# Optimization experiments

Measured on AMD Instinct MI355X. Metric: run time of the kernel, lower is better.

The kernel has to match this reference:

```python
import jax, jax.numpy as jnp
import numpy as np

B, T, D_IN, H, N_LAYERS, D_OUT = 256, 512, 128, 512, 3, 1


def setup_inputs() -> dict:
    key = jax.random.key(0)
    ks = jax.random.split(key, 20)
    s = 1.0 / np.sqrt(H)
    inp = {"x": jax.random.normal(ks[0], (B, T, D_IN), dtype=jnp.float32)}
    k = 1
    for l in range(N_LAYERS):
        d_in = D_IN if l == 0 else H
        inp[f"W_ih_{l}"] = jax.random.uniform(ks[k], (4 * H, d_in), minval=-s, maxval=s); k += 1
        inp[f"W_hh_{l}"] = jax.random.uniform(ks[k], (4 * H, H), minval=-s, maxval=s); k += 1
        inp[f"b_ih_{l}"] = jax.random.uniform(ks[k], (4 * H,), minval=-s, maxval=s); k += 1
        inp[f"b_hh_{l}"] = jax.random.uniform(ks[k], (4 * H,), minval=-s, maxval=s); k += 1
    inp["W_fc"] = jax.random.uniform(ks[k], (D_OUT, H), minval=-s, maxval=s); k += 1
    inp["b_fc"] = jax.random.uniform(ks[k], (D_OUT,), minval=-s, maxval=s)
    return inp


def _lstm_layer(x, W_ih, W_hh, b_ih, b_hh):
    # x: [B, T, d_in] -> hs: [B, T, H]. PyTorch gate order: i, f, g, o.
    xg = jnp.einsum("btd,gd->btg", x, W_ih) + b_ih + b_hh  # precompute input proj [B,T,4H]
    Hh = W_hh.shape[1]
    Bb = x.shape[0]

    def step(carry, xg_t):
        h, c = carry
        g = xg_t + h @ W_hh.T  # [B, 4H]
        i, f, gg, o = jnp.split(g, 4, axis=-1)
        c = jax.nn.sigmoid(f) * c + jax.nn.sigmoid(i) * jnp.tanh(gg)
        h = jax.nn.sigmoid(o) * jnp.tanh(c)
        return (h, c), h

    h0 = jnp.zeros((Bb, Hh), x.dtype)
    (_, _), hs = jax.lax.scan(step, (h0, h0), jnp.swapaxes(xg, 0, 1))
    return jnp.swapaxes(hs, 0, 1)


def reference(x, W_ih_0, W_hh_0, b_ih_0, b_hh_0,
              W_ih_1, W_hh_1, b_ih_1, b_hh_1,
              W_ih_2, W_hh_2, b_ih_2, b_hh_2,
              W_fc, b_fc):
    # Eval mode: inter-layer dropout (p=0.4) is identity.
    h = _lstm_layer(x, W_ih_0, W_hh_0, b_ih_0, b_hh_0)
    h = _lstm_layer(h, W_ih_1, W_hh_1, b_ih_1, b_hh_1)
    h = _lstm_layer(h, W_ih_2, W_hh_2, b_ih_2, b_hh_2)
    return h[:, -1, :] @ W_fc.T + b_fc  # [B, D_OUT]
```

## Files before the change

### kernel.cpp

```cpp
#include <hip/hip_runtime.h>

#define B_   256
#define T_   512
#define DIN_ 128
#define H_   512
#define G4_  2048

typedef __bf16 bf16_t;
typedef __bf16 bf16x8 __attribute__((ext_vector_type(8)));
typedef __bf16 bf16x4 __attribute__((ext_vector_type(4)));
typedef float  f32x4  __attribute__((ext_vector_type(4)));
typedef float  f32x16 __attribute__((ext_vector_type(16)));

__device__ __forceinline__ void gload16cc(const void* g, void* l) {
  __builtin_amdgcn_global_load_lds(
      (const __attribute__((address_space(1))) unsigned int*)g,
      (__attribute__((address_space(3))) unsigned int*)l, 16, 0, 17);
}

__global__ void cast_f32_bf16(const float* __restrict__ s, bf16_t* __restrict__ d, int n) {
  int i = (blockIdx.x * 256 + threadIdx.x) * 4;
  if (i >= n) return;
  float4 v = *(const float4*)(s + i);
  bf16x4 o;
  o[0] = (bf16_t)v.x; o[1] = (bf16_t)v.y; o[2] = (bf16_t)v.z; o[3] = (bf16_t)v.w;
  *(bf16x4*)(d + i) = o;
}

__global__ void cast_strided(const float* __restrict__ s, bf16_t* __restrict__ d,
                             int Ks, int Kd, int coff) {
  int npr = Ks >> 3;
  int i = blockIdx.x * 256 + threadIdx.x;
  if (i >= 2048 * npr) return;
  int row = i / npr, j = i - row * npr;
  const float* sp = s + (size_t)row * Ks + j * 8;
  float4 v0 = *(const float4*)sp;
  float4 v1 = *(const float4*)(sp + 4);
  bf16x8 o;
  o[0] = (bf16_t)v0.x; o[1] = (bf16_t)v0.y; o[2] = (bf16_t)v0.z; o[3] = (bf16_t)v0.w;
  o[4] = (bf16_t)v1.x; o[5] = (bf16_t)v1.y; o[6] = (bf16_t)v1.z; o[7] = (bf16_t)v1.w;
  *(bf16x8*)(d + (size_t)row * Kd + coff + j * 8) = o;
}

__global__ void bias_sum(const float* __restrict__ a, const float* __restrict__ b,
                         float* __restrict__ o, int n) {
  int i = blockIdx.x * 256 + threadIdx.x;
  if (i < n) o[i] = a[i] + b[i];
}

#define RING_N (8 * 256 * 512)
#define FSTR   16

template<bool L0>
__device__ __forceinline__ void step_loop(
    char* smem, const bf16_t* __restrict__ xbf, const bf16_t* __restrict__ wcl,
    const float* __restrict__ bias_l, bf16_t* ringPrev, bf16_t* ringOwn,
    float* __restrict__ hsf, int* flags, int layer, int bg, int ug)
{
  constexpr int KL   = L0 ? 640 : 1024;
  constexpr int ROWB = KL * 2;
  constexpr int XT   = L0 ? 4 : 16;
  constexpr int HT   = 16;
  constexpr int XP1  = L0 ? 2 : 8;
  constexpr int HOFF = L0 ? 256 : 1024;
  const int tid  = threadIdx.x;
  const int lane = tid & 63;
  const int wv   = tid >> 6;
  const int g    = wv & 3;
  const int kh   = wv >> 2;
  const int r32  = lane & 31;
  const int l5   = lane >> 5;
  const int u0   = ug * 32;
  const int t0x  = L0 ? (kh * 4) : (kh * 16);
  const int t0h  = L0 ? (8 + kh * 16) : (32 + kh * 16);

  bf16x8 wfrag[XT + HT];
  {
    const bf16_t* wrow = wcl + (size_t)(g * 512 + u0 + r32) * KL + l5 * 8;
    #pragma unroll
    for (int i = 0; i < XT; ++i) wfrag[i]      = *(const bf16x8*)(wrow + (t0x + i) * 16);
    #pragma unroll
    for (int i = 0; i < HT; ++i) wfrag[XT + i] = *(const bf16x8*)(wrow + (t0h + i) * 16);
  }
  const int um = tid >> 3;
  const int uq = tid & 7;
  float bsv[4][4];
  #pragma unroll
  for (int g2 = 0; g2 < 4; ++g2)
    #pragma unroll
    for (int q = 0; q < 4; ++q)
      bsv[g2][q] = bias_l[g2 * 512 + u0 + uq * 4 + q];

  float cst[4] = {0.f, 0.f, 0.f, 0.f};
  float* gp = (float*)smem;

  int* fl_own  = flags + ((layer * 512) * 4 + bg) * FSTR;
  int* fl_prev = flags + (((layer - 1) * 512) * 4 + bg) * FSTR;
  int* fl_next = flags + (((layer + 1) * 512) * 4 + bg) * FSTR;

  for (int s = 0; s < 512; ++s) {
    const int slot  = s & 7;
    const int slot2 = (s - 1) & 7;
    if (!L0) {
      if (tid == 0)
        while (__hip_atomic_load(fl_prev + s * 4 * FSTR, __ATOMIC_RELAXED,
                                 __HIP_MEMORY_SCOPE_AGENT) < 16)
          __builtin_amdgcn_s_sleep(1);
      __syncthreads();
      const bf16_t* prvS = ringPrev + (size_t)slot * (256 * 512) + (size_t)(bg * 64) * 512;
      #pragma unroll
      for (int i = 0; i < 8; ++i) {
        int r = i * 8 + wv;
        gload16cc(prvS + r * 512 + (lane ^ (r & 15)) * 8, smem + r * ROWB);
      }
    } else {
      #pragma unroll
      for (int i2 = 0; i2 < 2; ++i2) {
        int idx = i2 * 512 + tid;
        int r = idx >> 4, cx = idx & 15;
        int px = cx ^ (r & 15);
        bf16x8 v = *(const bf16x8*)(xbf + ((size_t)(bg * 64 + r) * T_ + s) * 128 + cx * 8);
        *(bf16x8*)(smem + r * ROWB + px * 16) = v;
      }
    }
    __syncthreads();
    f32x16 acc0 = {}, acc1 = {};
    #pragma unroll
    for (int i = 0; i < XP1; ++i) {
      const int px = ((t0x + i) * 2 + l5) ^ (r32 & 15);
      bf16x8 a0 = *(const bf16x8*)(smem + r32 * ROWB + px * 16);
      bf16x8 a1 = *(const bf16x8*)(smem + (32 + r32) * ROWB + px * 16);
      acc0 = __builtin_amdgcn_mfma_f32_32x32x16_bf16(a0, wfrag[i], acc0, 0, 0, 0);
      acc1 = __builtin_amdgcn_mfma_f32_32x32x16_bf16(a1, wfrag[i], acc1, 0, 0, 0);
    }
    if (tid == 0) {
      if (s > 0)
        while (__hip_atomic_load(fl_own + (s - 1) * 4 * FSTR, __ATOMIC_RELAXED,
                                 __HIP_MEMORY_SCOPE_AGENT) < 16)
          __builtin_amdgcn_s_sleep(1);
      if (layer < 2 && s >= 8)
        while (__hip_atomic_load(fl_next + (s - 8) * 4 * FSTR, __ATOMIC_RELAXED,
                                 __HIP_MEMORY_SCOPE_AGENT) < 16)
          __builtin_amdgcn_s_sleep(1);
    }
    __syncthreads();
    {
      const bf16_t* ownS = ringOwn + (size_t)slot2 * (256 * 512) + (size_t)(bg * 64) * 512;
      #pragma unroll
      for (int i = 0; i < 8; ++i) {
        int r = i * 8 + wv;
        gload16cc(ownS + r * 512 + (lane ^ (r & 15)) * 8, smem + r * ROWB + HOFF);
      }
    }
    #pragma unroll
    for (int i = XP1; i < XT; ++i) {
      const int px = ((t0x + i) * 2 + l5) ^ (r32 & 15);
      bf16x8 a0 = *(const bf16x8*)(smem + r32 * ROWB + px * 16);
      bf16x8 a1 = *(const bf16x8*)(smem + (32 + r32) * ROWB + px * 16);
      acc0 = __builtin_amdgcn_mfma_f32_32x32x16_bf16(a0, wfrag[i], acc0, 0, 0, 0);
      acc1 = __builtin_amdgcn_mfma_f32_32x32x16_bf16(a1, wfrag[i], acc1, 0, 0, 0);
    }
    __syncthreads();
    #pragma unroll
    for (int i = 0; i < HT; ++i) {
      const int px = ((t0h + i) * 2 + l5) ^ (r32 & 15);
      bf16x8 a0 = *(const bf16x8*)(smem + r32 * ROWB + px * 16);
      bf16x8 a1 = *(const bf16x8*)(smem + (32 + r32) * ROWB + px * 16);
      acc0 = __builtin_amdgcn_mfma_f32_32x32x16_bf16(a0, wfrag[XT + i], acc0, 0, 0, 0);
      acc1 = __builtin_amdgcn_mfma_f32_32x32x16_bf16(a1, wfrag[XT + i], acc1, 0, 0, 0);
    }
    __syncthreads();
    {
      const int base = kh * 8192 + g * 32 + r32;
      #pragma unroll
      for (int reg = 0; reg < 16; ++reg) {
        int mr = (reg & 3) + 8 * (reg >> 2) + 4 * l5;
        gp[base + mr * 128]        = acc0[reg];
        gp[base + (32 + mr) * 128] = acc1[reg];
      }
    }
    __syncthreads();
    union { bf16x4 v; unsigned long long u; } pk;
    f32x4 hvf;
    {
      f32x4 gv[4];
      #pragma unroll
      for (int g2 = 0; g2 < 4; ++g2) {
        f32x4 p0 = *(const f32x4*)&gp[um * 128 + g2 * 32 + uq * 4];
        f32x4 p1 = *(const f32x4*)&gp[8192 + um * 128 + g2 * 32 + uq * 4];
        #pragma unroll
        for (int q = 0; q < 4; ++q) gv[g2][q] = p0[q] + p1[q];
      }
      #pragma unroll
      for (int q = 0; q < 4; ++q) {
        float i_ = gv[0][q] + bsv[0][q];
        float f_ = gv[1][q] + bsv[1][q];
        float g_ = gv[2][q] + bsv[2][q];
        float o_ = gv[3][q] + bsv[3][q];
        float si = 1.f / (1.f + __expf(-i_));
        float sf = 1.f / (1.f + __expf(-f_));
        float so = 1.f / (1.f + __expf(-o_));
        float tg = 2.f / (1.f + __expf(-2.f * g_)) - 1.f;
        float cv = sf * cst[q] + si * tg;
        cst[q] = cv;
        float th = 2.f / (1.f + __expf(-2.f * cv)) - 1.f;
        hvf[q] = so * th;
        pk.v[q] = (bf16_t)hvf[q];
      }
    }
    {
      int b = bg * 64 + um;
      bf16_t* dst = ringOwn + (size_t)slot * (256 * 512) + (size_t)b * 512 + u0 + uq * 4;
      (void)__hip_atomic_exchange((unsigned long long*)dst, pk.u,
                                  __ATOMIC_RELAXED, __HIP_MEMORY_SCOPE_AGENT);
      if (layer == 2 && s == 511)
        *(f32x4*)(hsf + (size_t)b * 512 + u0 + uq * 4) = hvf;
    }
    __syncthreads();
    if (tid == 0)
      atomicAdd(fl_own + s * 4 * FSTR, 1);
  }
}

__global__ __launch_bounds__(512, 2)
void lstm_persist(const bf16_t* __restrict__ xbf, const bf16_t* __restrict__ wc,
                  const float* __restrict__ bias, bf16_t* __restrict__ rings,
                  float* __restrict__ hsf, int* __restrict__ flags)
{
  __shared__ __align__(16) char smem[131072];
  const int bid   = blockIdx.x;
  const int layer = bid >> 6;
  const int bg    = (bid >> 4) & 3;
  const int ug    = bid & 15;
  bf16_t* ringOwn  = rings + (size_t)layer * RING_N;
  bf16_t* ringPrev = rings + (size_t)(layer - 1) * RING_N;
  if (layer == 0) {
    step_loop<true>(smem, xbf, wc, bias, ringPrev, ringOwn, hsf, flags, 0, bg, ug);
  } else {
    const bf16_t* wcl = wc + 2048 * 640 + (size_t)(layer - 1) * 2048 * 1024;
    step_loop<false>(smem, xbf, wcl, bias + layer * 2048, ringPrev, ringOwn, hsf,
                     flags, layer, bg, ug);
  }
}

__global__ void fc_kernel(const float* __restrict__ h, const float* __restrict__ Wfc,
                          const float* __restrict__ bfc, float* __restrict__ out) {
  int b = blockIdx.x;
  int l = threadIdx.x;
  const float* hp = h + (size_t)b * H_;
  float acc = 0.f;
  #pragma unroll
  for (int i = 0; i < 8; ++i) acc += hp[l + i * 64] * Wfc[l + i * 64];
  #pragma unroll
  for (int off = 32; off; off >>= 1) acc += __shfl_down(acc, off, 64);
  if (l == 0) out[b] = acc + bfc[0];
}

extern "C" void kernel_launch(void* const* d_in, const int* in_sizes, int n_in,
                              void* d_out, int out_size, void* d_ws, size_t ws_size,
                              hipStream_t stream) {
  const float* x        = (const float*)d_in[0];
  const float* Wih_f[3] = {(const float*)d_in[1], (const float*)d_in[5], (const float*)d_in[9]};
  const float* Whh_f[3] = {(const float*)d_in[2], (const float*)d_in[6], (const float*)d_in[10]};
  const float* bih_f[3] = {(const float*)d_in[3], (const float*)d_in[7], (const float*)d_in[11]};
  const float* bhh_f[3] = {(const float*)d_in[4], (const float*)d_in[8], (const float*)d_in[12]};
  const float* Wfc = (const float*)d_in[13];
  const float* bfc = (const float*)d_in[14];

  char* ws = (char*)d_ws;
  size_t off = 0;
  auto take = [&](size_t bytes) { char* p = ws + off; off = (off + bytes + 255) & ~255ULL; return p; };
  bf16_t* XBF   = (bf16_t*)take((size_t)B_ * T_ * DIN_ * 2);
  bf16_t* WC    = (bf16_t*)take((size_t)(2048*640 + 2*2048*1024) * 2);
  float*  BIAS  = (float*) take(3 * 2048 * 4);
  bf16_t* RINGS = (bf16_t*)take((size_t)3 * RING_N * 2);
  float*  HSF   = (float*) take((size_t)B_ * H_ * 4);
  int*    FLAGS = (int*)   take(3 * 512 * 4 * FSTR * 4);

  bf16_t* WC1 = WC + 2048 * 640;
  bf16_t* WC2 = WC1 + 2048 * 1024;

  cast_f32_bf16<<<16384, 256, 0, stream>>>(x, XBF, B_ * T_ * DIN_);
  cast_strided<<<128, 256, 0, stream>>>(Wih_f[0], WC,  128, 640, 0);
  cast_strided<<<512, 256, 0, stream>>>(Whh_f[0], WC,  512, 640, 128);
  cast_strided<<<512, 256, 0, stream>>>(Wih_f[1], WC1, 512, 1024, 0);
  cast_strided<<<512, 256, 0, stream>>>(Whh_f[1], WC1, 512, 1024, 512);
  cast_strided<<<512, 256, 0, stream>>>(Wih_f[2], WC2, 512, 1024, 0);
  cast_strided<<<512, 256, 0, stream>>>(Whh_f[2], WC2, 512, 1024, 512);
  for (int l = 0; l < 3; ++l)
    bias_sum<<<8, 256, 0, stream>>>(bih_f[l], bhh_f[l], BIAS + l * 2048, G4_);
  hipMemsetAsync(RINGS, 0, (size_t)3 * RING_N * 2, stream);
  hipMemsetAsync(FLAGS, 0, 3 * 512 * 4 * FSTR * 4, stream);

  lstm_persist<<<192, 512, 0, stream>>>(XBF, WC, BIAS, RINGS, HSF, FLAGS);
  fc_kernel<<<B_, 64, 0, stream>>>(HSF, Wfc, bfc, (float*)d_out);
}
```

Before: 3.276 ms.

## Offload layer 1-2 input projections to helper blocks feeding fp32 xg rings

```diff
diff --git a/kernel.cpp b/kernel.cpp
--- a/kernel.cpp
+++ b/kernel.cpp
@@ -16,6 +16,9 @@
   __builtin_amdgcn_global_load_lds(
       (const __attribute__((address_space(1))) unsigned int*)g,
       (__attribute__((address_space(3))) unsigned int*)l, 16, 0, 17);
+}
+__device__ __forceinline__ int fload(const int* p) {
+  return __hip_atomic_load(p, __ATOMIC_RELAXED, __HIP_MEMORY_SCOPE_AGENT);
 }
 
 __global__ void cast_f32_bf16(const float* __restrict__ s, bf16_t* __restrict__ d, int n) {
@@ -49,20 +52,15 @@
 }
 
 #define RING_N (8 * 256 * 512)
+#define XG_N   (8 * 256 * 2048)
 #define FSTR   16
 
-template<bool L0>
-__device__ __forceinline__ void step_loop(
+__device__ __forceinline__ void l0_loop(
     char* smem, const bf16_t* __restrict__ xbf, const bf16_t* __restrict__ wcl,
-    const float* __restrict__ bias_l, bf16_t* ringPrev, bf16_t* ringOwn,
-    float* __restrict__ hsf, int* flags, int layer, int bg, int ug)
+    const float* __restrict__ bias_l, bf16_t* ringOwn, int* flags, int* xgf,
+    int bg, int ug)
 {
-  constexpr int KL   = L0 ? 640 : 1024;
-  constexpr int ROWB = KL * 2;
-  constexpr int XT   = L0 ? 4 : 16;
-  constexpr int HT   = 16;
-  constexpr int XP1  = L0 ? 2 : 8;
-  constexpr int HOFF = L0 ? 256 : 1024;
+  constexpr int ROWB = 1280;
   const int tid  = threadIdx.x;
   const int lane = tid & 63;
   const int wv   = tid >> 6;
@@ -71,16 +69,16 @@
   const int r32  = lane & 31;
   const int l5   = lane >> 5;
   const int u0   = ug * 32;
-  const int t0x  = L0 ? (kh * 4) : (kh * 16);
-  const int t0h  = L0 ? (8 + kh * 16) : (32 + kh * 16);
-
-  bf16x8 wfrag[XT + HT];
+  const int t0x  = kh * 4;
+  const int t0h  = 8 + kh * 16;
+
+  bf16x8 wfrag[20];
   {
-    const bf16_t* wrow = wcl + (size_t)(g * 512 + u0 + r32) * KL + l5 * 8;
-    #pragma unroll
-    for (int i = 0; i < XT; ++i) wfrag[i]      = *(const bf16x8*)(wrow + (t0x + i) * 16);
-    #pragma unroll
-    for (int i = 0; i < HT; ++i) wfrag[XT + i] = *(const bf16x8*)(wrow + (t0h + i) * 16);
+    const bf16_t* wrow = wcl + (size_t)(g * 512 + u0 + r32) * 640 + l5 * 8;
+    #pragma unroll
+    for (int i = 0; i < 4; ++i)  wfrag[i]     = *(const bf16x8*)(wrow + (t0x + i) * 16);
+    #pragma unroll
+    for (int i = 0; i < 16; ++i) wfrag[4 + i] = *(const bf16x8*)(wrow + (t0h + i) * 16);
   }
   const int um = tid >> 3;
   const int uq = tid & 7;
@@ -94,39 +92,24 @@
   float cst[4] = {0.f, 0.f, 0.f, 0.f};
   float* gp = (float*)smem;
 
-  int* fl_own  = flags + ((layer * 512) * 4 + bg) * FSTR;
-  int* fl_prev = flags + (((layer - 1) * 512) * 4 + bg) * FSTR;
-  int* fl_next = flags + (((layer + 1) * 512) * 4 + bg) * FSTR;
+  int* fl_own = flags + (0 * 4 + bg) * FSTR;
+  int* bpf    = xgf + (0 * 4 + bg) * FSTR;
 
   for (int s = 0; s < 512; ++s) {
     const int slot  = s & 7;
     const int slot2 = (s - 1) & 7;
-    if (!L0) {
-      if (tid == 0)
-        while (__hip_atomic_load(fl_prev + s * 4 * FSTR, __ATOMIC_RELAXED,
-                                 __HIP_MEMORY_SCOPE_AGENT) < 16)
-          __builtin_amdgcn_s_sleep(1);
-      __syncthreads();
-      const bf16_t* prvS = ringPrev + (size_t)slot * (256 * 512) + (size_t)(bg * 64) * 512;
-      #pragma unroll
-      for (int i = 0; i < 8; ++i) {
-        int r = i * 8 + wv;
-        gload16cc(prvS + r * 512 + (lane ^ (r & 15)) * 8, smem + r * ROWB);
-      }
-    } else {
-      #pragma unroll
-      for (int i2 = 0; i2 < 2; ++i2) {
-        int idx = i2 * 512 + tid;
-        int r = idx >> 4, cx = idx & 15;
-        int px = cx ^ (r & 15);
-        bf16x8 v = *(const bf16x8*)(xbf + ((size_t)(bg * 64 + r) * T_ + s) * 128 + cx * 8);
-        *(bf16x8*)(smem + r * ROWB + px * 16) = v;
-      }
+    {
+      int r0 = tid >> 4, c0 = tid & 15;
+      bf16x8 v0 = *(const bf16x8*)(xbf + ((size_t)(bg * 64 + r0) * T_ + s) * 128 + c0 * 8);
+      int i1 = 512 + tid, r1 = i1 >> 4, c1 = i1 & 15;
+      bf16x8 v1 = *(const bf16x8*)(xbf + ((size_t)(bg * 64 + r1) * T_ + s) * 128 + c1 * 8);
+      *(bf16x8*)(smem + r0 * ROWB + (c0 ^ (r0 & 15)) * 16) = v0;
+      *(bf16x8*)(smem + r1 * ROWB + (c1 ^ (r1 & 15)) * 16) = v1;
     }
     __syncthreads();
     f32x16 acc0 = {}, acc1 = {};
     #pragma unroll
-    for (int i = 0; i < XP1; ++i) {
+    for (int i = 0; i < 2; ++i) {
       const int px = ((t0x + i) * 2 + l5) ^ (r32 & 15);
       bf16x8 a0 = *(const bf16x8*)(smem + r32 * ROWB + px * 16);
       bf16x8 a1 = *(const bf16x8*)(smem + (32 + r32) * ROWB + px * 16);
@@ -135,13 +118,9 @@
     }
     if (tid == 0) {
       if (s > 0)
-        while (__hip_atomic_load(fl_own + (s - 1) * 4 * FSTR, __ATOMIC_RELAXED,
-                                 __HIP_MEMORY_SCOPE_AGENT) < 16)
-          __builtin_amdgcn_s_sleep(1);
-      if (layer < 2 && s >= 8)
-        while (__hip_atomic_load(fl_next + (s - 8) * 4 * FSTR, __ATOMIC_RELAXED,
-                                 __HIP_MEMORY_SCOPE_AGENT) < 16)
-          __builtin_amdgcn_s_sleep(1);
+        while (fload(fl_own + (s - 1) * 4 * FSTR) < 16) __builtin_amdgcn_s_sleep(1);
+      if (s >= 8)
+        while (fload(bpf + (s - 8) * 4 * FSTR) < 8) __builtin_amdgcn_s_sleep(1);
     }
     __syncthreads();
     {
@@ -149,11 +128,11 @@
       #pragma unroll
       for (int i = 0; i < 8; ++i) {
         int r = i * 8 + wv;
-        gload16cc(ownS + r * 512 + (lane ^ (r & 15)) * 8, smem + r * ROWB + HOFF);
-      }
-    }
-    #pragma unroll
-    for (int i = XP1; i < XT; ++i) {
+        gload16cc(ownS + r * 512 + (lane ^ (r & 15)) * 8, smem + r * ROWB + 256);
+      }
+    }
+    #pragma unroll
+    for (int i = 2; i < 4; ++i) {
       const int px = ((t0x + i) * 2 + l5) ^ (r32 & 15);
       bf16x8 a0 = *(const bf16x8*)(smem + r32 * ROWB + px * 16);
       bf16x8 a1 = *(const bf16x8*)(smem + (32 + r32) * ROWB + px * 16);
@@ -162,12 +141,12 @@
     }
     __syncthreads();
     #pragma unroll
-    for (int i = 0; i < HT; ++i) {
+    for (int i = 0; i < 16; ++i) {
       const int px = ((t0h + i) * 2 + l5) ^ (r32 & 15);
       bf16x8 a0 = *(const bf16x8*)(smem + r32 * ROWB + px * 16);
       bf16x8 a1 = *(const bf16x8*)(smem + (32 + r32) * ROWB + px * 16);
-      acc0 = __builtin_amdgcn_mfma_f32_32x32x16_bf16(a0, wfrag[XT + i], acc0, 0, 0, 0);
-      acc1 = __builtin_amdgcn_mfma_f32_32x32x16_bf16(a1, wfrag[XT + i], acc1, 0, 0, 0);
+      acc0 = __builtin_amdgcn_mfma_f32_32x32x16_bf16(a0, wfrag[4 + i], acc0, 0, 0, 0);
+      acc1 = __builtin_amdgcn_mfma_f32_32x32x16_bf16(a1, wfrag[4 + i], acc1, 0, 0, 0);
     }
     __syncthreads();
     {
@@ -181,7 +160,6 @@
     }
     __syncthreads();
     union { bf16x4 v; unsigned long long u; } pk;
-    f32x4 hvf;
     {
       f32x4 gv[4];
       #pragma unroll
@@ -204,6 +182,131 @@
         float cv = sf * cst[q] + si * tg;
         cst[q] = cv;
         float th = 2.f / (1.f + __expf(-2.f * cv)) - 1.f;
+        pk.v[q] = (bf16_t)(so * th);
+      }
+    }
+    {
+      int b = bg * 64 + um;
+      bf16_t* dst = ringOwn + (size_t)slot * (256 * 512) + (size_t)b * 512 + u0 + uq * 4;
+      (void)__hip_atomic_exchange((unsigned long long*)dst, pk.u,
+                                  __ATOMIC_RELAXED, __HIP_MEMORY_SCOPE_AGENT);
+    }
+    __syncthreads();
+    if (tid == 0) atomicAdd(fl_own + s * 4 * FSTR, 1);
+  }
+}
+
+__device__ __forceinline__ void main_loop(
+    char* smem, const bf16_t* __restrict__ wcl, const float* __restrict__ bias_l,
+    const float* __restrict__ xgRing, bf16_t* ringOwn, float* __restrict__ hsf,
+    int* flags, int* xgf, int layer, int bg, int ug)
+{
+  const int tid  = threadIdx.x;
+  const int lane = tid & 63;
+  const int wv   = tid >> 6;
+  const int g    = wv & 3;
+  const int kh   = wv >> 2;
+  const int r32  = lane & 31;
+  const int l5   = lane >> 5;
+  const int u0   = ug * 32;
+
+  bf16x8 wfrag[16];
+  {
+    const bf16_t* wrow = wcl + (size_t)(g * 512 + u0 + r32) * 1024 + 512 + kh * 256 + l5 * 8;
+    #pragma unroll
+    for (int i = 0; i < 16; ++i) wfrag[i] = *(const bf16x8*)(wrow + i * 16);
+  }
+  const int um = tid >> 3;
+  const int uq = tid & 7;
+  float bsv[4][4];
+  #pragma unroll
+  for (int g2 = 0; g2 < 4; ++g2)
+    #pragma unroll
+    for (int q = 0; q < 4; ++q)
+      bsv[g2][q] = bias_l[g2 * 512 + u0 + uq * 4 + q];
+
+  float cst[4] = {0.f, 0.f, 0.f, 0.f};
+
+  int* fl_own = flags + ((layer * 512) * 4 + bg) * FSTR;
+  int* xgf_in = xgf + (((layer - 1) * 512) * 4 + bg) * FSTR;
+  int* xgf_bp = xgf + ((1 * 512) * 4 + bg) * FSTR;
+
+  for (int s = 0; s < 512; ++s) {
+    const int slot  = s & 7;
+    const int slot2 = (s - 1) & 7;
+    if (tid == 0) {
+      while (fload(xgf_in + s * 4 * FSTR) < 8) __builtin_amdgcn_s_sleep(1);
+      if (s > 0)
+        while (fload(fl_own + (s - 1) * 4 * FSTR) < 16) __builtin_amdgcn_s_sleep(1);
+      if (layer == 1 && s >= 8)
+        while (fload(xgf_bp + (s - 8) * 4 * FSTR) < 8) __builtin_amdgcn_s_sleep(1);
+    }
+    __syncthreads();
+    {
+      const bf16_t* ownS = ringOwn + (size_t)slot2 * (256 * 512) + (size_t)(bg * 64) * 512;
+      #pragma unroll
+      for (int i = 0; i < 8; ++i) {
+        int r = i * 8 + wv;
+        gload16cc(ownS + r * 512 + (lane ^ (r & 15)) * 8, smem + r * 1024);
+      }
+      const float* xgS = xgRing + (size_t)slot * (256 * 2048) + (size_t)(bg * 64) * 2048;
+      #pragma unroll
+      for (int i = 0; i < 4; ++i) {
+        int id = (i * 8 + wv) * 64 + lane;
+        int row = id >> 5, sub = id & 31, g2 = sub >> 3, cp = sub & 7;
+        gload16cc(xgS + (size_t)row * 2048 + g2 * 512 + u0 + cp * 4,
+                  smem + 65536 + (i * 8 + wv) * 1024);
+      }
+    }
+    __syncthreads();
+    f32x16 acc0 = {}, acc1 = {};
+    #pragma unroll
+    for (int i = 0; i < 16; ++i) {
+      const int c  = (kh * 16 + i) * 2 + l5;
+      const int px = c ^ (r32 & 15);
+      bf16x8 a0 = *(const bf16x8*)(smem + r32 * 1024 + px * 16);
+      bf16x8 a1 = *(const bf16x8*)(smem + (32 + r32) * 1024 + px * 16);
+      acc0 = __builtin_amdgcn_mfma_f32_32x32x16_bf16(a0, wfrag[i], acc0, 0, 0, 0);
+      acc1 = __builtin_amdgcn_mfma_f32_32x32x16_bf16(a1, wfrag[i], acc1, 0, 0, 0);
+    }
+    __syncthreads();
+    {
+      char* pb = smem + kh * 32768 + (g * 32 + r32) * 4;
+      #pragma unroll
+      for (int reg = 0; reg < 16; ++reg) {
+        int mr = (reg & 3) + 8 * (reg >> 2) + 4 * l5;
+        *(float*)(pb + mr * 512)        = acc0[reg];
+        *(float*)(pb + (32 + mr) * 512) = acc1[reg];
+      }
+    }
+    __syncthreads();
+    union { bf16x4 v; unsigned long long u; } pk;
+    f32x4 hvf;
+    {
+      const char* gpb = smem + um * 512;
+      const char* xgb = smem + 65536 + um * 512;
+      f32x4 gvv[4];
+      #pragma unroll
+      for (int g2 = 0; g2 < 4; ++g2) {
+        f32x4 p0 = *(const f32x4*)(gpb + (g2 * 32 + uq * 4) * 4);
+        f32x4 p1 = *(const f32x4*)(gpb + 32768 + (g2 * 32 + uq * 4) * 4);
+        f32x4 xv = *(const f32x4*)(xgb + g2 * 128 + uq * 16);
+        #pragma unroll
+        for (int q = 0; q < 4; ++q) gvv[g2][q] = p0[q] + p1[q] + xv[q];
+      }
+      #pragma unroll
+      for (int q = 0; q < 4; ++q) {
+        float i_ = gvv[0][q] + bsv[0][q];
+        float f_ = gvv[1][q] + bsv[1][q];
+        float g_ = gvv[2][q] + bsv[2][q];
+        float o_ = gvv[3][q] + bsv[3][q];
+        float si = 1.f / (1.f + __expf(-i_));
+        float sf = 1.f / (1.f + __expf(-f_));
+        float so = 1.f / (1.f + __expf(-o_));
+        float tg = 2.f / (1.f + __expf(-2.f * g_)) - 1.f;
+        float cv = sf * cst[q] + si * tg;
+        cst[q] = cv;
+        float th = 2.f / (1.f + __expf(-2.f * cv)) - 1.f;
         hvf[q] = so * th;
         pk.v[q] = (bf16_t)hvf[q];
       }
@@ -217,29 +320,104 @@
         *(f32x4*)(hsf + (size_t)b * 512 + u0 + uq * 4) = hvf;
     }
     __syncthreads();
-    if (tid == 0)
-      atomicAdd(fl_own + s * 4 * FSTR, 1);
+    if (tid == 0) atomicAdd(fl_own + s * 4 * FSTR, 1);
+  }
+}
+
+__device__ __forceinline__ void helper_loop(
+    char* smem, const bf16_t* __restrict__ wihl, const bf16_t* __restrict__ ringPrev,
+    float* __restrict__ xgRing, int* flags, int* xgf, int hl, int bg, int ng)
+{
+  const int tid  = threadIdx.x;
+  const int lane = tid & 63;
+  const int wv   = tid >> 6;
+  const int r32  = lane & 31;
+  const int l5   = lane >> 5;
+  const int n0   = ng * 256 + wv * 32;
+
+  bf16x8 wfrag[32];
+  {
+    const bf16_t* wrow = wihl + (size_t)(n0 + r32) * 1024 + l5 * 8;
+    #pragma unroll
+    for (int i = 0; i < 32; ++i) wfrag[i] = *(const bf16x8*)(wrow + i * 16);
+  }
+  int* fl_prev = flags + (((hl - 1) * 512) * 4 + bg) * FSTR;
+  int* fl_cons = flags + ((hl * 512) * 4 + bg) * FSTR;
+  int* xgf_own = xgf + (((hl - 1) * 512) * 4 + bg) * FSTR;
+
+  for (int s = 0; s < 512; ++s) {
+    const int slot = s & 7;
+    if (tid == 0) {
+      while (fload(fl_prev + s * 4 * FSTR) < 16) __builtin_amdgcn_s_sleep(1);
+      if (s >= 8)
+        while (fload(fl_cons + (s - 8) * 4 * FSTR) < 16) __builtin_amdgcn_s_sleep(1);
+    }
+    __syncthreads();
+    {
+      const bf16_t* src = ringPrev + (size_t)slot * (256 * 512) + (size_t)(bg * 64) * 512;
+      #pragma unroll
+      for (int i = 0; i < 8; ++i) {
+        int r = i * 8 + wv;
+        gload16cc(src + r * 512 + (lane ^ (r & 15)) * 8, smem + r * 1024);
+      }
+    }
+    __syncthreads();
+    f32x16 acc0 = {}, acc1 = {};
+    #pragma unroll
+    for (int i = 0; i < 32; ++i) {
+      const int px = (i * 2 + l5) ^ (r32 & 15);
+      bf16x8 a0 = *(const bf16x8*)(smem + r32 * 1024 + px * 16);
+      bf16x8 a1 = *(const bf16x8*)(smem + (32 + r32) * 1024 + px * 16);
+      acc0 = __builtin_amdgcn_mfma_f32_32x32x16_bf16(a0, wfrag[i], acc0, 0, 0, 0);
+      acc1 = __builtin_amdgcn_mfma_f32_32x32x16_bf16(a1, wfrag[i], acc1, 0, 0, 0);
+    }
+    {
+      float* dst = xgRing + (size_t)slot * (256 * 2048) + (size_t)(bg * 64) * 2048 + n0 + r32;
+      #pragma unroll
+      for (int reg = 0; reg < 16; ++reg) {
+        int mr = (reg & 3) + 8 * (reg >> 2) + 4 * l5;
+        __hip_atomic_store(dst + (size_t)mr * 2048, acc0[reg],
+                           __ATOMIC_RELAXED, __HIP_MEMORY_SCOPE_AGENT);
+        __hip_atomic_store(dst + (size_t)(32 + mr) * 2048, acc1[reg],
+                           __ATOMIC_RELAXED, __HIP_MEMORY_SCOPE_AGENT);
+      }
+    }
+    __syncthreads();
+    if (tid == 0) atomicAdd(xgf_own + s * 4 * FSTR, 1);
   }
 }
 
 __global__ __launch_bounds__(512, 2)
 void lstm_persist(const bf16_t* __restrict__ xbf, const bf16_t* __restrict__ wc,
                   const float* __restrict__ bias, bf16_t* __restrict__ rings,
-                  float* __restrict__ hsf, int* __restrict__ flags)
+                  float* __restrict__ xg, float* __restrict__ hsf,
+                  int* __restrict__ flags)
 {
   __shared__ __align__(16) char smem[131072];
-  const int bid   = blockIdx.x;
-  const int layer = bid >> 6;
-  const int bg    = (bid >> 4) & 3;
-  const int ug    = bid & 15;
-  bf16_t* ringOwn  = rings + (size_t)layer * RING_N;
-  bf16_t* ringPrev = rings + (size_t)(layer - 1) * RING_N;
-  if (layer == 0) {
-    step_loop<true>(smem, xbf, wc, bias, ringPrev, ringOwn, hsf, flags, 0, bg, ug);
+  int* xgf = flags + 3 * 512 * 4 * FSTR;
+  const int bid = blockIdx.x;
+  if (bid < 192) {
+    const int layer = bid >> 6;
+    const int bg    = (bid >> 4) & 3;
+    const int ug    = bid & 15;
+    bf16_t* ringOwn = rings + (size_t)layer * RING_N;
+    if (layer == 0) {
+      l0_loop(smem, xbf, wc, bias, ringOwn, flags, xgf, bg, ug);
+    } else {
+      const bf16_t* wcl = wc + 2048 * 640 + (size_t)(layer - 1) * 2048 * 1024;
+      const float* xgR  = xg + (size_t)(layer - 1) * XG_N;
+      main_loop(smem, wcl, bias + layer * 2048, xgR, ringOwn, hsf, flags, xgf,
+                layer, bg, ug);
+    }
   } else {
-    const bf16_t* wcl = wc + 2048 * 640 + (size_t)(layer - 1) * 2048 * 1024;
-    step_loop<false>(smem, xbf, wcl, bias + layer * 2048, ringPrev, ringOwn, hsf,
-                     flags, layer, bg, ug);
+    const int hid = bid - 192;
+    const int hl  = 1 + (hid >> 5);
+    const int bg  = (hid >> 3) & 3;
+    const int ng  = hid & 7;
+    const bf16_t* wihl = wc + 2048 * 640 + (size_t)(hl - 1) * 2048 * 1024;
+    const bf16_t* ringPrev = rings + (size_t)(hl - 1) * RING_N;
+    float* xgR = xg + (size_t)(hl - 1) * XG_N;
+    helper_loop(smem, wihl, ringPrev, xgR, flags, xgf, hl, bg, ng);
   }
 }
 
@@ -267,6 +445,8 @@
   const float* Wfc = (const float*)d_in[13];
   const float* bfc = (const float*)d_in[14];
 
+  const size_t FLAGS_BYTES = (size_t)(3 * 512 * 4 + 2 * 512 * 4) * FSTR * 4;
+
   char* ws = (char*)d_ws;
   size_t off = 0;
   auto take = [&](size_t bytes) { char* p = ws + off; off = (off + bytes + 255) & ~255ULL; return p; };
@@ -274,8 +454,9 @@
   bf16_t* WC    = (bf16_t*)take((size_t)(2048*640 + 2*2048*1024) * 2);
   float*  BIAS  = (float*) take(3 * 2048 * 4);
   bf16_t* RINGS = (bf16_t*)take((size_t)3 * RING_N * 2);
+  float*  XG    = (float*) take((size_t)2 * XG_N * 4);
   float*  HSF   = (float*) take((size_t)B_ * H_ * 4);
-  int*    FLAGS = (int*)   take(3 * 512 * 4 * FSTR * 4);
+  int*    FLAGS = (int*)   take(FLAGS_BYTES);
 
   bf16_t* WC1 = WC + 2048 * 640;
   bf16_t* WC2 = WC1 + 2048 * 1024;
@@ -290,8 +471,8 @@
   for (int l = 0; l < 3; ++l)
     bias_sum<<<8, 256, 0, stream>>>(bih_f[l], bhh_f[l], BIAS + l * 2048, G4_);
   hipMemsetAsync(RINGS, 0, (size_t)3 * RING_N * 2, stream);
-  hipMemsetAsync(FLAGS, 0, 3 * 512 * 4 * FSTR * 4, stream);
-
-  lstm_persist<<<192, 512, 0, stream>>>(XBF, WC, BIAS, RINGS, HSF, FLAGS);
+  hipMemsetAsync(FLAGS, 0, FLAGS_BYTES, stream);
+
+  lstm_persist<<<256, 512, 0, stream>>>(XBF, WC, BIAS, RINGS, XG, HSF, FLAGS);
   fc_kernel<<<B_, 64, 0, stream>>>(HSF, Wfc, bfc, (float*)d_out);
 }
```

Result: no change. 3.311 ms (+1.1%).
